# Performance work log

Measured on AMD Instinct MI355X. Metric: run time of the kernel, lower is better.

Reference implementation:

```python
import jax, jax.numpy as jnp
import numpy as np

IN_FEATURES = 2048
OUT_FEATURES = 2048
BATCH = 32768
EPS = 1e-10

def setup_inputs() -> dict:
    key = jax.random.key(0)
    kx, kp = jax.random.split(key)
    x = jax.random.normal(kx, (BATCH, IN_FEATURES), dtype=jnp.float32)
    P = jax.random.normal(kp, (OUT_FEATURES, IN_FEATURES), dtype=jnp.float32)
    bias = jnp.zeros((OUT_FEATURES,), dtype=jnp.float32)
    return {"x": x, "P": P, "bias": bias}

def reference(x, P, bias):
    # Gram matrix of columns of P: [in, in]
    PTP = jnp.abs(P.T @ P)
    # per-column (dim=0 sum) AOL rescaling factor: [in]
    d = 1.0 / jnp.sqrt(PTP.sum(axis=0) + EPS)
    # W = P @ diag(d) == column-wise scale of P
    W = P * d[None, :]          # [out, in]
    return x @ W.T + bias        # [batch, out]
```

## Files before the change

### kernel.cpp

```cpp
#include <hip/hip_runtime.h>
#include <hip/hip_bf16.h>
#include <stdint.h>

#define IN_F  2048
#define OUT_F 2048
#define BATCH 32768

typedef __attribute__((ext_vector_type(8))) short  short8;
typedef __attribute__((ext_vector_type(4))) float  floatx4;

static constexpr int LDT = 32;
static constexpr int TILE_USH = 128 * LDT;

__device__ __forceinline__ uint16_t f2bf(float f) {
  union { float f; uint32_t u; } v; v.f = f;
  uint32_t r = v.u + 0x7FFFu + ((v.u >> 16) & 1u);
  return (uint16_t)(r >> 16);
}

__device__ __forceinline__ void gl_lds16(const uint16_t* g, uint16_t* l) {
  __builtin_amdgcn_global_load_lds(
      (const __attribute__((address_space(1))) unsigned int*)(g),
      (__attribute__((address_space(3))) unsigned int*)(l), 16, 0, 0);
}

__device__ __forceinline__ void gemm128_pipeline(
    const uint16_t* __restrict__ A, const uint16_t* __restrict__ B,
    int bm, int bn, int K, uint16_t* sA, uint16_t* sB,
    floatx4 (&acc)[4][4]) {
  const int tid  = threadIdx.x;
  const int wave = tid >> 6, lane = tid & 63;
  const int wm = (wave >> 1) * 64, wn = (wave & 1) * 64;

  const int r0   = wave * 32 + (lane >> 2);
  const int scol = (lane & 3) * 8;
  const uint16_t* gA = A + (size_t)(bm + r0) * K + scol;
  const uint16_t* gB = B + (size_t)(bn + r0) * K + scol;
  const size_t rowK16 = (size_t)16 * K;

  const int ch0 = wave * 2 * (16 * LDT);
  const int ch1 = ch0 + 16 * LDT;

  const int ra = (wm + (lane & 15)) * LDT + (lane >> 4) * 8;
  const int rb = (wn + (lane & 15)) * LDT + (lane >> 4) * 8;

  gl_lds16(gA,          sA + ch0);
  gl_lds16(gA + rowK16, sA + ch1);
  gl_lds16(gB,          sB + ch0);
  gl_lds16(gB + rowK16, sB + ch1);
  gA += 32; gB += 32;
  __syncthreads();

  const int NK = K / 32;
  int p = 0;
  for (int k = 0; k < NK; k++, p ^= 1) {
    if (k + 1 < NK) {
      const int q = (p ^ 1) * TILE_USH;
      gl_lds16(gA,          sA + q + ch0);
      gl_lds16(gA + rowK16, sA + q + ch1);
      gl_lds16(gB,          sB + q + ch0);
      gl_lds16(gB + rowK16, sB + q + ch1);
      gA += 32; gB += 32;
    }
    const uint16_t* cA = sA + p * TILE_USH;
    const uint16_t* cB = sB + p * TILE_USH;
    short8 af[4], bf[4];
#pragma unroll
    for (int i = 0; i < 4; i++) {
      af[i] = *(const short8*)&cA[ra + i * 16 * LDT];
      bf[i] = *(const short8*)&cB[rb + i * 16 * LDT];
    }
#pragma unroll
    for (int i = 0; i < 4; i++)
#pragma unroll
      for (int j = 0; j < 4; j++)
        acc[i][j] = __builtin_amdgcn_mfma_f32_16x16x32_bf16(af[i], bf[j], acc[i][j], 0, 0, 0);
    __syncthreads();
  }
}

__global__ __launch_bounds__(256) void k_prep(
    const float* __restrict__ P, uint16_t* __restrict__ PT,
    uint16_t* __restrict__ PB) {
  __shared__ float tile[32][33];
  const int bx = blockIdx.x * 32;
  const int by = blockIdx.y * 32;
  const int tx = threadIdx.x & 31;
  const int ty = threadIdx.x >> 5;
#pragma unroll
  for (int i = 0; i < 32; i += 8) {
    float v = P[(size_t)(by + ty + i) * IN_F + bx + tx];
    tile[ty + i][tx] = v;
    PB[(size_t)(by + ty + i) * IN_F + bx + tx] = f2bf(v);
  }
  __syncthreads();
#pragma unroll
  for (int i = 0; i < 32; i += 8)
    PT[(size_t)(bx + ty + i) * IN_F + by + tx] = f2bf(tile[tx][ty + i]);
}

__global__ __launch_bounds__(256) void k_gram_colsum(
    const uint16_t* __restrict__ PT, float* __restrict__ colsum) {
  __shared__ __align__(16) uint16_t sA[2 * TILE_USH];
  __shared__ __align__(16) uint16_t sB[2 * TILE_USH];
  __shared__ float colpart[128];

  const int tid = threadIdx.x;
  const int wave = tid >> 6, lane = tid & 63;
  const int bm = blockIdx.x * 128, bn = blockIdx.y * 128;
  const int wn = (wave & 1) * 64;

  floatx4 z = {0.f, 0.f, 0.f, 0.f};
  floatx4 acc[4][4];
#pragma unroll
  for (int i = 0; i < 4; i++)
#pragma unroll
    for (int j = 0; j < 4; j++) acc[i][j] = z;

  gemm128_pipeline(PT, PT, bm, bn, OUT_F, sA, sB, acc);

  if (tid < 128) colpart[tid] = 0.f;
  __syncthreads();
#pragma unroll
  for (int j = 0; j < 4; j++) {
    float s = 0.f;
#pragma unroll
    for (int i = 0; i < 4; i++)
#pragma unroll
      for (int r = 0; r < 4; r++) s += fabsf(acc[i][j][r]);
    atomicAdd(&colpart[wn + j * 16 + (lane & 15)], s);
  }
  __syncthreads();
  if (tid < 128) atomicAdd(&colsum[bn + tid], colpart[tid]);
}

__global__ void k_finalize_d(const float* __restrict__ colsum, float* __restrict__ dv) {
  int i = blockIdx.x * blockDim.x + threadIdx.x;
  if (i < IN_F) dv[i] = 1.0f / sqrtf(colsum[i] + 1e-10f);
}

__global__ __launch_bounds__(256) void k_cvt_x(
    const float4* __restrict__ X4, const float4* __restrict__ dv4,
    uint4* __restrict__ XB) {
  size_t t = (size_t)blockIdx.x * 256 + threadIdx.x;
  int c4 = (int)((2 * t) & (IN_F / 4 - 1));
  float4 a = X4[2 * t], b = X4[2 * t + 1];
  float4 d0 = dv4[c4], d1 = dv4[c4 + 1];
  uint4 o;
  o.x = (uint32_t)f2bf(a.x * d0.x) | ((uint32_t)f2bf(a.y * d0.y) << 16);
  o.y = (uint32_t)f2bf(a.z * d0.z) | ((uint32_t)f2bf(a.w * d0.w) << 16);
  o.z = (uint32_t)f2bf(b.x * d1.x) | ((uint32_t)f2bf(b.y * d1.y) << 16);
  o.w = (uint32_t)f2bf(b.z * d1.z) | ((uint32_t)f2bf(b.w * d1.w) << 16);
  XB[t] = o;
}

__global__ __launch_bounds__(256) void k_gemm_nt(
    const uint16_t* __restrict__ A,
    const uint16_t* __restrict__ B,
    const float* __restrict__ bias,
    float* __restrict__ C) {
  __shared__ __align__(16) uint16_t sA[2 * TILE_USH];
  __shared__ __align__(16) uint16_t sB[2 * TILE_USH];

  const int tid = threadIdx.x;
  const int wave = tid >> 6, lane = tid & 63;
  const int bm = blockIdx.y * 128;
  const int bn = blockIdx.x * 128;
  const int wm = (wave >> 1) * 64, wn = (wave & 1) * 64;

  floatx4 z = {0.f, 0.f, 0.f, 0.f};
  floatx4 acc[4][4];
#pragma unroll
  for (int i = 0; i < 4; i++)
#pragma unroll
    for (int j = 0; j < 4; j++) acc[i][j] = z;

  gemm128_pipeline(A, B, bm, bn, IN_F, sA, sB, acc);

#pragma unroll
  for (int j = 0; j < 4; j++) {
    const int col = bn + wn + j * 16 + (lane & 15);
    const float bv = bias[col];
#pragma unroll
    for (int i = 0; i < 4; i++) {
      const int row0 = bm + wm + i * 16 + (lane >> 4) * 4;
#pragma unroll
      for (int r = 0; r < 4; r++)
        C[(size_t)(row0 + r) * OUT_F + col] = acc[i][j][r] + bv;
    }
  }
}

__global__ __launch_bounds__(256) void fb_gram(const float* __restrict__ P,
                                               float* __restrict__ colsum) {
  __shared__ float red[256];
  const int j = blockIdx.x;
  float s = 0.f;
  for (int i = threadIdx.x; i < IN_F; i += 256) {
    float dot = 0.f;
    for (int k = 0; k < OUT_F; k++)
      dot = fmaf(P[(size_t)k * IN_F + i], P[(size_t)k * IN_F + j], dot);
    s += fabsf(dot);
  }
  red[threadIdx.x] = s;
  __syncthreads();
  for (int st = 128; st > 0; st >>= 1) {
    if (threadIdx.x < st) red[threadIdx.x] += red[threadIdx.x + st];
    __syncthreads();
  }
  if (threadIdx.x == 0) colsum[j] = red[0];
}

__global__ __launch_bounds__(256) void fb_gemm(
    const float* __restrict__ X, const float* __restrict__ P,
    const float* __restrict__ dv, const float* __restrict__ bias,
    float* __restrict__ out) {
  __shared__ __align__(16) float xs[64][20];
  __shared__ __align__(16) float ps[64][20];
  const int bm = blockIdx.x * 64, bn = blockIdx.y * 64;
  const int tx = threadIdx.x & 15, ty = threadIdx.x >> 4;
  float acc[4][4] = {};
  const int r = threadIdx.x >> 2, kc = (threadIdx.x & 3) * 4;
  for (int k0 = 0; k0 < IN_F; k0 += 16) {
    float4 xv = *(const float4*)&X[(size_t)(bm + r) * IN_F + k0 + kc];
    float4 pv = *(const float4*)&P[(size_t)(bn + r) * IN_F + k0 + kc];
    float4 dd = *(const float4*)&dv[k0 + kc];
    float4 pw; pw.x = pv.x * dd.x; pw.y = pv.y * dd.y; pw.z = pv.z * dd.z; pw.w = pv.w * dd.w;
    *(float4*)&xs[r][kc] = xv;
    *(float4*)&ps[r][kc] = pw;
    __syncthreads();
#pragma unroll
    for (int kk = 0; kk < 16; kk++) {
      float a0[4], b0[4];
#pragma unroll
      for (int i = 0; i < 4; i++) a0[i] = xs[ty * 4 + i][kk];
#pragma unroll
      for (int jj = 0; jj < 4; jj++) b0[jj] = ps[tx * 4 + jj][kk];
#pragma unroll
      for (int i = 0; i < 4; i++)
#pragma unroll
        for (int jj = 0; jj < 4; jj++) acc[i][jj] = fmaf(a0[i], b0[jj], acc[i][jj]);
    }
    __syncthreads();
  }
#pragma unroll
  for (int i = 0; i < 4; i++)
#pragma unroll
    for (int jj = 0; jj < 4; jj++) {
      int row = bm + ty * 4 + i, col = bn + tx * 4 + jj;
      out[(size_t)row * OUT_F + col] = acc[i][jj] + bias[col];
    }
}

extern "C" void kernel_launch(void* const* d_in, const int* in_sizes, int n_in,
                              void* d_out, int out_size, void* d_ws, size_t ws_size,
                              hipStream_t stream) {
  const float* x    = (const float*)d_in[0];
  const float* P    = (const float*)d_in[1];
  const float* bias = (const float*)d_in[2];
  float* out = (float*)d_out;
  char* ws = (char*)d_ws;

  const size_t SZ_PT = (size_t)IN_F * OUT_F * 2;
  const size_t SZ_PB = (size_t)IN_F * OUT_F * 2;
  const size_t SZ_XB = (size_t)BATCH * IN_F * 2;
  const size_t need  = SZ_PT + SZ_PB + SZ_XB + 2 * IN_F * sizeof(float) + 256;

  if (ws_size >= need) {
    uint16_t* PT = (uint16_t*)ws;
    uint16_t* PB = (uint16_t*)(ws + SZ_PT);
    uint16_t* XB = (uint16_t*)(ws + SZ_PT + SZ_PB);
    float* colsum = (float*)(ws + SZ_PT + SZ_PB + SZ_XB);
    float* dv = colsum + IN_F;

    hipMemsetAsync(colsum, 0, IN_F * sizeof(float), stream);
    k_prep<<<dim3(64, 64), 256, 0, stream>>>(P, PT, PB);
    k_gram_colsum<<<dim3(16, 16), 256, 0, stream>>>(PT, colsum);
    k_finalize_d<<<8, 256, 0, stream>>>(colsum, dv);
    k_cvt_x<<<(int)(((size_t)BATCH * IN_F / 8) / 256), 256, 0, stream>>>(
        (const float4*)x, (const float4*)dv, (uint4*)XB);
    k_gemm_nt<<<dim3(OUT_F / 128, BATCH / 128), 256, 0, stream>>>(XB, PB, bias, out);
  } else {
    float* colsum = (float*)ws;
    float* dv = colsum + IN_F;
    fb_gram<<<IN_F, 256, 0, stream>>>(P, colsum);
    k_finalize_d<<<8, 256, 0, stream>>>(colsum, dv);
    fb_gemm<<<dim3(BATCH / 64, OUT_F / 64), 256, 0, stream>>>(x, P, dv, bias, out);
  }
}
```

Before: 833.8 us.

## Rewrite main GEMM with 256x128 tiles, triple-buffered LDS, swizzle, and XCD remap

Replaces the 128x128, 256-thread main GEMM with a 256x128-tile, 512-thread kernel that uses BK=64 and a three-stage LDS ring fed by global_load_lds. Loads for stage t+2 are interleaved with the MFMA work on stage t. LDS rows get an XOR swizzle to avoid bank conflicts, a 1D grid is remapped so neighbouring tiles land on the same XCD for L2 reuse, and setprio is raised around the MFMA bursts. The aim is to hide memory latency and raise MFMA utilisation. In exchange, LDS use and barriers per iteration go up, and the hand-counted vmcnt waits must match the real load counts.

Result: slower. 854.0 us (+2.4%).

```diff
diff --git a/kernel.cpp b/kernel.cpp
--- a/kernel.cpp
+++ b/kernel.cpp
@@ -11,6 +11,13 @@
 
 static constexpr int LDT = 32;
 static constexpr int TILE_USH = 128 * LDT;
+
+#define BM 256
+#define BN 128
+#define BK 64
+#define NKT (IN_F / BK)
+#define A_TILE_USH (BM * BK)
+#define B_TILE_USH (BN * BK)
 
 __device__ __forceinline__ uint16_t f2bf(float f) {
   union { float f; uint32_t u; } v; v.f = f;
@@ -154,28 +161,122 @@
   XB[t] = o;
 }
 
-__global__ __launch_bounds__(256) void k_gemm_nt(
+__global__ __launch_bounds__(512, 2) void k_gemm_nt(
     const uint16_t* __restrict__ A,
     const uint16_t* __restrict__ B,
     const float* __restrict__ bias,
     float* __restrict__ C) {
-  __shared__ __align__(16) uint16_t sA[2 * TILE_USH];
-  __shared__ __align__(16) uint16_t sB[2 * TILE_USH];
-
-  const int tid = threadIdx.x;
-  const int wave = tid >> 6, lane = tid & 63;
-  const int bm = blockIdx.y * 128;
-  const int bn = blockIdx.x * 128;
-  const int wm = (wave >> 1) * 64, wn = (wave & 1) * 64;
-
-  floatx4 z = {0.f, 0.f, 0.f, 0.f};
+  __shared__ __align__(16) uint16_t sA[3 * A_TILE_USH];
+  __shared__ __align__(16) uint16_t sB[3 * B_TILE_USH];
+
+  const int tid  = threadIdx.x;
+  const int lane = tid & 63, wid = tid >> 6;
+
+  const int lin = blockIdx.x;
+  const int x   = (lin & 7) * 256 + (lin >> 3);
+  const int bn  = (x & 15) * BN;
+  const int bm  = (x >> 4) * BM;
+
+  const int wm = (wid >> 1) * 64;
+  const int wn = (wid & 1) * 64;
+
+  const int nA0 = 0 * 512 + tid, nA1 = 1 * 512 + tid, nA2 = 2 * 512 + tid, nA3 = 3 * 512 + tid;
+  const int nB0 = 0 * 512 + tid, nB1 = 1 * 512 + tid;
+#define SRC_OFF(n) ((size_t)(((n) >> 3)) * IN_F + ((((n) & 7) ^ (((n) >> 3) & 7)) * 8))
+  const uint16_t* gA0 = A + (size_t)bm * IN_F + SRC_OFF(nA0);
+  const uint16_t* gA1 = A + (size_t)bm * IN_F + SRC_OFF(nA1);
+  const uint16_t* gA2 = A + (size_t)bm * IN_F + SRC_OFF(nA2);
+  const uint16_t* gA3 = A + (size_t)bm * IN_F + SRC_OFF(nA3);
+  const uint16_t* gB0 = B + (size_t)bn * IN_F + SRC_OFF(nB0);
+  const uint16_t* gB1 = B + (size_t)bn * IN_F + SRC_OFF(nB1);
+#undef SRC_OFF
+  const int dA0 = (0 * 512 + wid * 64) * 8, dA1 = (1 * 512 + wid * 64) * 8;
+  const int dA2 = (2 * 512 + wid * 64) * 8, dA3 = (3 * 512 + wid * 64) * 8;
+  const int dB0 = (0 * 512 + wid * 64) * 8, dB1 = (1 * 512 + wid * 64) * 8;
+
+  const int rsw0 = (((lane >> 4) + 0) ^ (lane & 7)) * 8;
+  const int rsw1 = (((lane >> 4) + 4) ^ (lane & 7)) * 8;
+  const int raBase = (wm + (lane & 15)) * BK;
+  const int rbBase = (wn + (lane & 15)) * BK;
+
+  floatx4 zz = {0.f, 0.f, 0.f, 0.f};
   floatx4 acc[4][4];
 #pragma unroll
   for (int i = 0; i < 4; i++)
 #pragma unroll
-    for (int j = 0; j < 4; j++) acc[i][j] = z;
-
-  gemm128_pipeline(A, B, bm, bn, IN_F, sA, sB, acc);
+    for (int j = 0; j < 4; j++) acc[i][j] = zz;
+
+  {
+    uint16_t* dA = sA;            uint16_t* dB = sB;
+    gl_lds16(gA0, dA + dA0); gl_lds16(gA1, dA + dA1);
+    gl_lds16(gA2, dA + dA2); gl_lds16(gA3, dA + dA3);
+    gl_lds16(gB0, dB + dB0); gl_lds16(gB1, dB + dB1);
+    gA0 += BK; gA1 += BK; gA2 += BK; gA3 += BK; gB0 += BK; gB1 += BK;
+    dA = sA + A_TILE_USH;         dB = sB + B_TILE_USH;
+    gl_lds16(gA0, dA + dA0); gl_lds16(gA1, dA + dA1);
+    gl_lds16(gA2, dA + dA2); gl_lds16(gA3, dA + dA3);
+    gl_lds16(gB0, dB + dB0); gl_lds16(gB1, dB + dB1);
+    gA0 += BK; gA1 += BK; gA2 += BK; gA3 += BK; gB0 += BK; gB1 += BK;
+  }
+  asm volatile("s_waitcnt vmcnt(6)" ::: "memory");
+  __builtin_amdgcn_s_barrier();
+
+  int rb = 0, wb = 2;
+  for (int t = 0; t < NKT; t++) {
+    const uint16_t* cA = sA + rb * A_TILE_USH;
+    const uint16_t* cB = sB + rb * B_TILE_USH;
+    uint16_t* dA = sA + wb * A_TILE_USH;
+    uint16_t* dB = sB + wb * B_TILE_USH;
+    const bool pf = (t + 2 < NKT);
+
+    short8 af[4], bf[4];
+#pragma unroll
+    for (int i = 0; i < 4; i++) af[i] = *(const short8*)&cA[raBase + i * 1024 + rsw0];
+#pragma unroll
+    for (int j = 0; j < 4; j++) bf[j] = *(const short8*)&cB[rbBase + j * 1024 + rsw0];
+    if (pf) {
+      gl_lds16(gA0, dA + dA0);
+      gl_lds16(gA1, dA + dA1);
+      gl_lds16(gB0, dB + dB0);
+    }
+    __builtin_amdgcn_s_barrier();
+    __builtin_amdgcn_s_setprio(1);
+#pragma unroll
+    for (int i = 0; i < 4; i++)
+#pragma unroll
+      for (int j = 0; j < 4; j++)
+        acc[i][j] = __builtin_amdgcn_mfma_f32_16x16x32_bf16(af[i], bf[j], acc[i][j], 0, 0, 0);
+    __builtin_amdgcn_s_setprio(0);
+    __builtin_amdgcn_s_barrier();
+
+#pragma unroll
+    for (int i = 0; i < 4; i++) af[i] = *(const short8*)&cA[raBase + i * 1024 + rsw1];
+#pragma unroll
+    for (int j = 0; j < 4; j++) bf[j] = *(const short8*)&cB[rbBase + j * 1024 + rsw1];
+    if (pf) {
+      gl_lds16(gA2, dA + dA2);
+      gl_lds16(gA3, dA + dA3);
+      gl_lds16(gB1, dB + dB1);
+      gA0 += BK; gA1 += BK; gA2 += BK; gA3 += BK; gB0 += BK; gB1 += BK;
+    }
+    __builtin_amdgcn_s_barrier();
+    __builtin_amdgcn_s_setprio(1);
+#pragma unroll
+    for (int i = 0; i < 4; i++)
+#pragma unroll
+      for (int j = 0; j < 4; j++)
+        acc[i][j] = __builtin_amdgcn_mfma_f32_16x16x32_bf16(af[i], bf[j], acc[i][j], 0, 0, 0);
+    __builtin_amdgcn_s_setprio(0);
+    if (t + 2 < NKT) {
+      asm volatile("s_waitcnt vmcnt(6)" ::: "memory");
+    } else if (t + 1 < NKT) {
+      asm volatile("s_waitcnt vmcnt(0)" ::: "memory");
+    }
+    __builtin_amdgcn_s_barrier();
+
+    rb = (rb == 2) ? 0 : rb + 1;
+    wb = (wb == 2) ? 0 : wb + 1;
+  }
 
 #pragma unroll
   for (int j = 0; j < 4; j++) {
@@ -279,7 +380,7 @@
     k_finalize_d<<<8, 256, 0, stream>>>(colsum, dv);
     k_cvt_x<<<(int)(((size_t)BATCH * IN_F / 8) / 256), 256, 0, stream>>>(
         (const float4*)x, (const float4*)dv, (uint4*)XB);
-    k_gemm_nt<<<dim3(OUT_F / 128, BATCH / 128), 256, 0, stream>>>(XB, PB, bias, out);
+    k_gemm_nt<<<(BATCH / BM) * (OUT_F / BN), 512, 0, stream>>>(XB, PB, bias, out);
   } else {
     float* colsum = (float*)ws;
     float* dv = colsum + IN_F;
```

## Rewrite main GEMM with 256x128x64 tiles, triple-buffered LDS and XCD-aware block mapping

Applied to the files above, without the earlier changes.

Replaces the 128x128 GEMM pipeline with a 512-thread block computing 256x128 tiles with BK=64. It triple-buffers A and B in LDS via direct global-to-LDS loads with an XOR swizzle to avoid bank conflicts. A linear block index is remapped so consecutive blocks land on the same XCD, and MFMA sections run under raised wave priority. The goal is more operand reuse per LDS byte, deeper latency hiding and better L2 locality, at the cost of larger LDS footprint (~144KB for two blocks) and more complex hand-unrolled scheduling.

New measurement: 819.2 us. No clear change (-1.7%).

```diff
diff --git a/kernel.cpp b/kernel.cpp
--- a/kernel.cpp
+++ b/kernel.cpp
@@ -11,6 +11,13 @@
 
 static constexpr int LDT = 32;
 static constexpr int TILE_USH = 128 * LDT;
+
+#define BM 256
+#define BN 128
+#define BK 64
+#define NKT (IN_F / BK)
+#define A_TILE_USH (BM * BK)
+#define B_TILE_USH (BN * BK)
 
 __device__ __forceinline__ uint16_t f2bf(float f) {
   union { float f; uint32_t u; } v; v.f = f;
@@ -154,28 +161,104 @@
   XB[t] = o;
 }
 
-__global__ __launch_bounds__(256) void k_gemm_nt(
+__global__ __launch_bounds__(512, 2) void k_gemm_nt(
     const uint16_t* __restrict__ A,
     const uint16_t* __restrict__ B,
     const float* __restrict__ bias,
     float* __restrict__ C) {
-  __shared__ __align__(16) uint16_t sA[2 * TILE_USH];
-  __shared__ __align__(16) uint16_t sB[2 * TILE_USH];
-
-  const int tid = threadIdx.x;
-  const int wave = tid >> 6, lane = tid & 63;
-  const int bm = blockIdx.y * 128;
-  const int bn = blockIdx.x * 128;
-  const int wm = (wave >> 1) * 64, wn = (wave & 1) * 64;
-
-  floatx4 z = {0.f, 0.f, 0.f, 0.f};
+  __shared__ __align__(16) uint16_t sA[3 * A_TILE_USH];
+  __shared__ __align__(16) uint16_t sB[3 * B_TILE_USH];
+
+  const int tid  = threadIdx.x;
+  const int lane = tid & 63, wid = tid >> 6;
+
+  const int lin = blockIdx.x;
+  const int x   = (lin & 7) * 256 + (lin >> 3);
+  const int bn  = (x & 15) * BN;
+  const int bm  = (x >> 4) * BM;
+
+  const int wm = (wid >> 1) * 64;
+  const int wn = (wid & 1) * 64;
+
+  const int nA0 = 0 * 512 + tid, nA1 = 1 * 512 + tid, nA2 = 2 * 512 + tid, nA3 = 3 * 512 + tid;
+  const int nB0 = 0 * 512 + tid, nB1 = 1 * 512 + tid;
+#define SRC_OFF(n) ((size_t)(((n) >> 3)) * IN_F + ((((n) & 7) ^ (((n) >> 3) & 7)) * 8))
+  const uint16_t* gA0 = A + (size_t)bm * IN_F + SRC_OFF(nA0);
+  const uint16_t* gA1 = A + (size_t)bm * IN_F + SRC_OFF(nA1);
+  const uint16_t* gA2 = A + (size_t)bm * IN_F + SRC_OFF(nA2);
+  const uint16_t* gA3 = A + (size_t)bm * IN_F + SRC_OFF(nA3);
+  const uint16_t* gB0 = B + (size_t)bn * IN_F + SRC_OFF(nB0);
+  const uint16_t* gB1 = B + (size_t)bn * IN_F + SRC_OFF(nB1);
+#undef SRC_OFF
+  const int dA0 = (0 * 512 + wid * 64) * 8, dA1 = (1 * 512 + wid * 64) * 8;
+  const int dA2 = (2 * 512 + wid * 64) * 8, dA3 = (3 * 512 + wid * 64) * 8;
+  const int dB0 = (0 * 512 + wid * 64) * 8, dB1 = (1 * 512 + wid * 64) * 8;
+
+  const int rsw0 = (((lane >> 4) + 0) ^ (lane & 7)) * 8;
+  const int rsw1 = (((lane >> 4) + 4) ^ (lane & 7)) * 8;
+  const int raBase = (wm + (lane & 15)) * BK;
+  const int rbBase = (wn + (lane & 15)) * BK;
+
+  floatx4 zz = {0.f, 0.f, 0.f, 0.f};
   floatx4 acc[4][4];
 #pragma unroll
   for (int i = 0; i < 4; i++)
 #pragma unroll
-    for (int j = 0; j < 4; j++) acc[i][j] = z;
-
-  gemm128_pipeline(A, B, bm, bn, IN_F, sA, sB, acc);
+    for (int j = 0; j < 4; j++) acc[i][j] = zz;
+
+  gl_lds16(gA0, sA + 0 * A_TILE_USH + dA0); gl_lds16(gA1, sA + 0 * A_TILE_USH + dA1);
+  gl_lds16(gA2, sA + 0 * A_TILE_USH + dA2); gl_lds16(gA3, sA + 0 * A_TILE_USH + dA3);
+  gl_lds16(gB0, sB + 0 * B_TILE_USH + dB0); gl_lds16(gB1, sB + 0 * B_TILE_USH + dB1);
+  gA0 += BK; gA1 += BK; gA2 += BK; gA3 += BK; gB0 += BK; gB1 += BK;
+  gl_lds16(gA0, sA + 1 * A_TILE_USH + dA0); gl_lds16(gA1, sA + 1 * A_TILE_USH + dA1);
+  gl_lds16(gA2, sA + 1 * A_TILE_USH + dA2); gl_lds16(gA3, sA + 1 * A_TILE_USH + dA3);
+  gl_lds16(gB0, sB + 1 * B_TILE_USH + dB0); gl_lds16(gB1, sB + 1 * B_TILE_USH + dB1);
+  gA0 += BK; gA1 += BK; gA2 += BK; gA3 += BK; gB0 += BK; gB1 += BK;
+  asm volatile("s_waitcnt vmcnt(6)" ::: "memory");
+  __builtin_amdgcn_s_barrier();
+
+#define TILE(RB, WB, PF, WAITN)                                               \
+  do {                                                                        \
+    const uint16_t* cA = sA + (RB) * A_TILE_USH;                              \
+    const uint16_t* cB = sB + (RB) * B_TILE_USH;                              \
+    if (PF) {                                                                 \
+      uint16_t* dA = sA + (WB) * A_TILE_USH;                                  \
+      uint16_t* dB = sB + (WB) * B_TILE_USH;                                  \
+      gl_lds16(gA0, dA + dA0); gl_lds16(gA1, dA + dA1);                       \
+      gl_lds16(gA2, dA + dA2); gl_lds16(gA3, dA + dA3);                       \
+      gl_lds16(gB0, dB + dB0); gl_lds16(gB1, dB + dB1);                       \
+      gA0 += BK; gA1 += BK; gA2 += BK; gA3 += BK; gB0 += BK; gB1 += BK;       \
+    }                                                                         \
+    short8 af0[4], bf0[4], af1[4], bf1[4];                                    \
+    _Pragma("unroll") for (int i = 0; i < 4; i++) {                           \
+      af0[i] = *(const short8*)&cA[raBase + i * 1024 + rsw0];                 \
+      af1[i] = *(const short8*)&cA[raBase + i * 1024 + rsw1];                 \
+    }                                                                         \
+    _Pragma("unroll") for (int j = 0; j < 4; j++) {                           \
+      bf0[j] = *(const short8*)&cB[rbBase + j * 1024 + rsw0];                 \
+      bf1[j] = *(const short8*)&cB[rbBase + j * 1024 + rsw1];                 \
+    }                                                                         \
+    __builtin_amdgcn_s_setprio(1);                                            \
+    _Pragma("unroll") for (int i = 0; i < 4; i++)                             \
+      _Pragma("unroll") for (int j = 0; j < 4; j++)                           \
+        acc[i][j] = __builtin_amdgcn_mfma_f32_16x16x32_bf16(af0[i], bf0[j], acc[i][j], 0, 0, 0); \
+    _Pragma("unroll") for (int i = 0; i < 4; i++)                             \
+      _Pragma("unroll") for (int j = 0; j < 4; j++)                           \
+        acc[i][j] = __builtin_amdgcn_mfma_f32_16x16x32_bf16(af1[i], bf1[j], acc[i][j], 0, 0, 0); \
+    __builtin_amdgcn_s_setprio(0);                                            \
+    if ((WAITN) == 6) asm volatile("s_waitcnt vmcnt(6)" ::: "memory");        \
+    if ((WAITN) == 0) asm volatile("s_waitcnt vmcnt(0)" ::: "memory");        \
+    if ((WAITN) >= 0) __builtin_amdgcn_s_barrier();                           \
+  } while (0)
+
+  for (int tt = 0; tt < 30; tt += 3) {
+    TILE(0, 2, true, 6);
+    TILE(1, 0, true, 6);
+    TILE(2, 1, true, 6);
+  }
+  TILE(0, 0, false, 0);
+  TILE(1, 0, false, -1);
+#undef TILE
 
 #pragma unroll
   for (int j = 0; j < 4; j++) {
@@ -279,7 +362,7 @@
     k_finalize_d<<<8, 256, 0, stream>>>(colsum, dv);
     k_cvt_x<<<(int)(((size_t)BATCH * IN_F / 8) / 256), 256, 0, stream>>>(
         (const float4*)x, (const float4*)dv, (uint4*)XB);
-    k_gemm_nt<<<dim3(OUT_F / 128, BATCH / 128), 256, 0, stream>>>(XB, PB, bias, out);
+    k_gemm_nt<<<(BATCH / BM) * (OUT_F / BN), 512, 0, stream>>>(XB, PB, bias, out);
   } else {
     float* colsum = (float*)ws;
     float* dv = colsum + IN_F;
```
